# Optimization experiments

Hardware: AMD Instinct MI355X
Metric: run time of the kernel (lower is better)

The kernel has to match this reference:

```python
import jax, jax.numpy as jnp
import numpy as np
import math

N, NP, D, H, W, HEADS = 4, 1024, 256, 64, 64, 8
DH = D // HEADS


def _norm_coords(height, width):
    # (height*width, 2) with (x, y) in [0, 1], row-major flatten (y outer, x inner)
    y = jnp.linspace(0.0, 1.0, height)
    x = jnp.linspace(0.0, 1.0, width)
    yg, xg = jnp.meshgrid(y, x, indexing='ij')
    return jnp.stack([xg.reshape(-1), yg.reshape(-1)], axis=-1)


def _pos_enc(coords, dim):
    # coords: (P, 2) -> (P, dim); even slots sin(x*div), odd slots cos(y*div)
    div = jnp.exp(jnp.arange(0, dim, 2, dtype=coords.dtype) * (-math.log(10000.0) / dim))
    s = jnp.sin(coords[:, 0:1] * div)  # (P, dim/2)
    c = jnp.cos(coords[:, 1:2] * div)  # (P, dim/2)
    return jnp.stack([s, c], axis=-1).reshape(coords.shape[0], dim)


def setup_inputs() -> dict:
    key = jax.random.key(0)
    ks = jax.random.split(key, 10)
    sc = 1.0 / math.sqrt(D)
    return {
        "local_feat": jax.random.normal(ks[0], (N, NP, D), jnp.float32),
        "global_feat": jax.random.normal(ks[1], (N, D, H, W), jnp.float32),
        "Wq": jax.random.normal(ks[2], (D, D), jnp.float32) * sc,
        "bq": jax.random.normal(ks[3], (D,), jnp.float32) * sc,
        "Wk": jax.random.normal(ks[4], (D, D), jnp.float32) * sc,
        "bk": jax.random.normal(ks[5], (D,), jnp.float32) * sc,
        "Wv": jax.random.normal(ks[6], (D, D), jnp.float32) * sc,
        "bv": jax.random.normal(ks[7], (D,), jnp.float32) * sc,
        "Wo": jax.random.normal(ks[8], (D, D), jnp.float32) * sc,
        "bo": jax.random.normal(ks[9], (D,), jnp.float32) * sc,
    }


def reference(local_feat, global_feat, Wq, bq, Wk, bk, Wv, bv, Wo, bo):
    n, N_p, d = local_feat.shape
    _, _, h, w = global_feat.shape
    hw = h * w
    P = int(math.sqrt(N_p))

    gf = jnp.transpose(global_feat.reshape(n, d, hw), (0, 2, 1))  # (n, HW, d)

    lf = local_feat + _pos_enc(_norm_coords(P, P), d)[None]       # (n, N_p, d)
    gf = gf + _pos_enc(_norm_coords(h, w), d)[None]               # (n, HW, d)

    q = (lf @ Wq.T + bq).reshape(n, N_p, HEADS, DH)
    k = (gf @ Wk.T + bk).reshape(n, hw, HEADS, DH)
    v = (gf @ Wv.T + bv).reshape(n, hw, HEADS, DH)

    scores = jnp.einsum('bqhd,bkhd->bhqk', q, k) / math.sqrt(DH)  # (n, H, N_p, HW)
    attn = jax.nn.softmax(scores, axis=-1)
    out = jnp.einsum('bhqk,bkhd->bqhd', attn, v).reshape(n, N_p, d)

    return (lf + out) @ Wo.T + bo
```

## Files before the change

kernel.cpp:

```cpp
#include <hip/hip_runtime.h>
#include <hip/hip_bf16.h>
#include <math.h>

#define NB    4
#define NPTS  1024
#define DD    256
#define HWW   4096
#define NHEAD 8
#define DHD   32
#define VTROW 4128

typedef short s8v  __attribute__((ext_vector_type(8)));
typedef float f4v  __attribute__((ext_vector_type(4)));
typedef float f4s  __attribute__((ext_vector_type(4)));
typedef unsigned int u2v __attribute__((ext_vector_type(2)));
typedef unsigned int u4v __attribute__((ext_vector_type(4)));

#define MFMA_BF16 __builtin_amdgcn_mfma_f32_16x16x32_bf16

#define PE_FACT (-9.210340371976184f / 256.0f)
#define QSCALE 0.2550348637f

__device__ __forceinline__ unsigned packbf(float hi, float lo) {
    return __builtin_amdgcn_perm(__float_as_uint(hi), __float_as_uint(lo), 0x07060302u);
}
__device__ __forceinline__ unsigned pack2rne(float lo, float hi) {
    __hip_bfloat16 a = __float2bfloat16(lo), b = __float2bfloat16(hi);
    return (unsigned)*(unsigned short*)&a | ((unsigned)*(unsigned short*)&b << 16);
}

__global__ __launch_bounds__(256) void prep(const float* __restrict__ lf,
                                            const float* __restrict__ gfeat,
                                            const float* __restrict__ wq,
                                            const float* __restrict__ wk,
                                            const float* __restrict__ wv,
                                            const float* __restrict__ wo,
                                            __hip_bfloat16* __restrict__ lf_pe_b,
                                            __hip_bfloat16* __restrict__ gf_pe_b,
                                            __hip_bfloat16* __restrict__ W4) {
    __shared__ float tile[32][33];
    int b = blockIdx.x, tid = threadIdx.x;
    if (b < 1024) {
        int idx4 = (b * 256 + tid) * 4;
        f4s f = *(const f4s*)(lf + idx4);
        int c = idx4 & 255;
        int p = (idx4 >> 8) & 1023;
        float x = (float)(p & 31) * (1.0f / 31.0f);
        float y = (float)(p >> 5) * (1.0f / 31.0f);
        float div0 = __expf((float)c * PE_FACT);
        float div2 = __expf((float)(c + 2) * PE_FACT);
        float e0 = f.x + __sinf(x * div0);
        float e1 = f.y + __cosf(y * div0);
        float e2 = f.z + __sinf(x * div2);
        float e3 = f.w + __cosf(y * div2);
        u2v o2 = { pack2rne(e0, e1), pack2rne(e2, e3) };
        *(u2v*)((unsigned*)lf_pe_b + (idx4 >> 1)) = o2;
    } else if (b < 5120) {
        int t = b - 1024;
        int n = t >> 10, r = t & 1023;
        int p0 = (r >> 3) * 32, c0 = (r & 7) * 32;
        int tx = tid & 31, ty = tid >> 5;
#pragma unroll
        for (int i = 0; i < 4; ++i)
            tile[ty + 8 * i][tx] = gfeat[((size_t)n * DD + (c0 + ty + 8 * i)) * HWW + p0 + tx];
        __syncthreads();
#pragma unroll
        for (int i = 0; i < 4; ++i) {
            int p = p0 + ty + 8 * i, c = c0 + tx;
            float div = __expf((float)(c & ~1) * PE_FACT);
            float pe = (c & 1) ? __cosf((float)(p >> 6) * (1.0f / 63.0f) * div)
                               : __sinf((float)(p & 63) * (1.0f / 63.0f) * div);
            gf_pe_b[((size_t)n * HWW + p) * DD + c] = __float2bfloat16(tile[tx][ty + 8 * i] + pe);
        }
    } else {
        int idx4 = ((b - 5120) * 256 + tid) * 4;
        int m = idx4 >> 16, r = idx4 & 65535;
        const float* src = (m == 0) ? wq : (m == 1) ? wk : (m == 2) ? wv : wo;
        f4s f = *(const f4s*)(src + r);
        u2v o2 = { pack2rne(f.x, f.y), pack2rne(f.z, f.w) };
        *(u2v*)((unsigned*)W4 + (idx4 >> 1)) = o2;
    }
}

__global__ __launch_bounds__(256, 2) void gemmQKV(const __hip_bfloat16* __restrict__ Aq,
                                                  const __hip_bfloat16* __restrict__ Akv,
                                                  const __hip_bfloat16* __restrict__ W4,
                                                  const float* __restrict__ bq,
                                                  const float* __restrict__ bk,
                                                  const float* __restrict__ bv,
                                                  __hip_bfloat16* __restrict__ Qb,
                                                  __hip_bfloat16* __restrict__ Kb,
                                                  __hip_bfloat16* __restrict__ Vtb) {
    __shared__ __align__(16) unsigned shbuf[2304];
    int tid = threadIdx.x;
    int wave = tid >> 6, lane = tid & 63;
    int quad = lane >> 4, c16 = lane & 15;
    int b = blockIdx.x;

    int typ, c0, mgrp, mstride;
    const short* Ap;
    const short* Wp;
    const float* bias;
    if (b < 128) {
        typ = 0; c0 = (b >> 5) * 64; mgrp = b & 31; mstride = 2048;
        Ap = (const short*)Aq; Wp = (const short*)W4; bias = bq;
    } else {
        int bb = b - 128;
        int combo = bb >> 7;
        mgrp = bb & 127; mstride = 8192;
        int mat = combo & 1;
        typ = 1 + mat;
        c0 = (combo >> 1) * 64;
        Ap = (const short*)Akv;
        Wp = (const short*)W4 + (1 + mat) * DD * DD;
        bias = mat ? bv : bk;
    }

    s8v w[8][4];
    const short* wp0 = Wp + (c0 + c16) * DD + quad * 8;
#pragma unroll
    for (int ks = 0; ks < 8; ++ks)
#pragma unroll
        for (int t = 0; t < 4; ++t)
            w[ks][t] = *(const s8v*)(wp0 + t * 16 * DD + ks * 32);
    float bvv[4];
#pragma unroll
    for (int t = 0; t < 4; ++t) bvv[t] = bias[c0 + t * 16 + c16];

    int mbase0 = mgrp * 64;
    int mbase1 = mbase0 + mstride;
    const short* ap0 = Ap + (mbase0 + wave * 16 + c16) * DD + quad * 8;
    const short* ap1 = Ap + (mbase1 + wave * 16 + c16) * DD + quad * 8;
    s8v a0[8], a1[8];
#pragma unroll
    for (int ks = 0; ks < 8; ++ks) a0[ks] = *(const s8v*)(ap0 + ks * 32);
#pragma unroll
    for (int ks = 0; ks < 8; ++ks) a1[ks] = *(const s8v*)(ap1 + ks * 32);

#pragma unroll
    for (int it = 0; it < 2; ++it) {
        int mbase = it ? mbase1 : mbase0;
        f4v acc[4];
#pragma unroll
        for (int t = 0; t < 4; ++t) acc[t] = (f4v){0.f, 0.f, 0.f, 0.f};
#pragma unroll
        for (int ks = 0; ks < 8; ++ks) {
            s8v a = it ? a1[ks] : a0[ks];
#pragma unroll
            for (int t = 0; t < 4; ++t)
                acc[t] = MFMA_BF16(a, w[ks][t], acc[t], 0, 0, 0);
        }

        if (typ != 2) {
            short* kt = (short*)shbuf;
            __syncthreads();
#pragma unroll
            for (int t = 0; t < 4; ++t) {
#pragma unroll
                for (int r = 0; r < 4; ++r) {
                    float v = acc[t][r] + bvv[t];
                    if (typ == 0) v *= QSCALE;
                    __hip_bfloat16 hv = __float2bfloat16(v);
                    kt[(wave * 16 + quad * 4 + r) * 72 + t * 16 + c16] = *(short*)&hv;
                }
            }
            __syncthreads();
            int pl  = tid >> 2;
            int seg = tid & 3;
            const short* src = kt + pl * 72 + seg * 16;
            u4v w0 = *(const u4v*)(src);
            u4v w1 = *(const u4v*)(src + 8);
            int h   = (c0 >> 5) + (seg >> 1);
            int dh0 = (seg & 1) * 16;
            short* dst;
            if (typ == 0) {
                int row = mbase + pl;
                int n = row >> 10, p = row & 1023;
                dst = (short*)Qb + (((size_t)(n * NHEAD + h) << 10) + p) * DHD + dh0;
            } else {
                int n = mbase >> 12, p = (mbase & 4095) + pl;
                dst = (short*)Kb + (((size_t)(n * NHEAD + h) << 12) + p) * DHD + dh0;
            }
            *(u4v*)(dst)     = w0;
            *(u4v*)(dst + 8) = w1;
        } else {
            unsigned (*stv)[36] = (unsigned (*)[36])shbuf;
            __syncthreads();
#pragma unroll
            for (int t = 0; t < 4; ++t) {
#pragma unroll
                for (int rp = 0; rp < 2; ++rp) {
                    __hip_bfloat16 lo = __float2bfloat16(acc[t][2 * rp] + bvv[t]);
                    __hip_bfloat16 hi = __float2bfloat16(acc[t][2 * rp + 1] + bvv[t]);
                    unsigned dw = (unsigned)*(unsigned short*)&lo |
                                  ((unsigned)*(unsigned short*)&hi << 16);
                    stv[t * 16 + c16][wave * 8 + quad * 2 + rp] = dw;
                }
            }
            __syncthreads();
            int col = tid >> 2;
            int kd  = (tid & 3) * 8;
            int grp = kd & 16;
            int ob  = kd & 15;
            unsigned vals[8];
#pragma unroll
            for (int i = 0; i < 8; ++i) {
                int o = ob + i;
                int idw = ((o >> 2) << 1) | (o & 1) | ((o & 2) << 2);
                vals[i] = stv[col][grp + idw];
            }
            int nblk = mbase >> 12;
            int kb   = mbase & 4095;
            int gh = (c0 + col) >> 5, gdh = (c0 + col) & 31;
            short* vp = (short*)Vtb + ((size_t)(nblk * NHEAD + gh) * DHD + gdh) * VTROW + kb + kd * 2;
            *(u4v*)(vp)     = (u4v){vals[0], vals[1], vals[2], vals[3]};
            *(u4v*)(vp + 8) = (u4v){vals[4], vals[5], vals[6], vals[7]};
        }
    }
}

template <int NC>
__global__ __launch_bounds__(256) void attn(const __hip_bfloat16* __restrict__ Q,
                                            const __hip_bfloat16* __restrict__ Kg,
                                            const __hip_bfloat16* __restrict__ Vt,
                                            __hip_bfloat16* __restrict__ Opart,
                                            float* __restrict__ lpart) {
    constexpr int CK = HWW / NC;
    constexpr int NSTEP = CK / 32;

    int tid = threadIdx.x;
    int wave = tid >> 6, lane = tid & 63;
    int quad = lane >> 4, c16 = lane & 15;

    int id = blockIdx.x;
    int xcd = id & 7;
    int s = id >> 3;
    int qtile = s & 3;
    int gidx = ((s >> 2) << 3) | xcd;
    int bh = gidx & 31;
    int chunk = gidx >> 5;

    int q0 = qtile * 256 + wave * 64;

    const short* Qs = (const short*)Q + (size_t)bh * NPTS * DHD;
    const short* Ks = (const short*)Kg + ((size_t)bh * HWW + (size_t)chunk * CK) * DHD;
    const short* Vs = (const short*)Vt + (size_t)bh * DHD * VTROW + (size_t)chunk * CK;

    s8v aq[4];
#pragma unroll
    for (int g = 0; g < 4; ++g)
        aq[g] = *(const s8v*)(Qs + (q0 + g * 16 + c16) * DHD + quad * 8);

    const f4v zf = {0.f, 0.f, 0.f, 0.f};
    f4v o[4][2];
#pragma unroll
    for (int g = 0; g < 4; ++g) { o[g][0] = zf; o[g][1] = zf; }
    float lsum[4] = {0.f, 0.f, 0.f, 0.f};

    const short* kbase  = Ks + c16 * DHD + quad * 8;
    const short* v0base = Vs + c16 * VTROW + quad * 8;
    const short* v1base = Vs + (16 + c16) * VTROW + quad * 8;

    s8v kfA = *(const s8v*)(kbase);
    s8v kfB = *(const s8v*)(kbase + 16 * DHD);
    s8v vfA = *(const s8v*)(v0base);
    s8v vfB = *(const s8v*)(v1base);

    for (int st = 0; st < NSTEP; ++st) {
        bool more = (st + 1) < NSTEP;
        s8v nkA, nkB, nvA, nvB;
        if (more) {
            int ko = (st + 1) * 32;
            nkA = *(const s8v*)(kbase + ko * DHD);
            nkB = *(const s8v*)(kbase + ko * DHD + 16 * DHD);
            nvA = *(const s8v*)(v0base + ko);
            nvB = *(const s8v*)(v1base + ko);
        }
#pragma unroll
        for (int g = 0; g < 4; ++g) {
            f4v sA = MFMA_BF16(kfA, aq[g], zf, 0, 0, 0);
            f4v sB = MFMA_BF16(kfB, aq[g], zf, 0, 0, 0);
            float pA0 = __builtin_amdgcn_exp2f(sA[0]);
            float pA1 = __builtin_amdgcn_exp2f(sA[1]);
            float pA2 = __builtin_amdgcn_exp2f(sA[2]);
            float pA3 = __builtin_amdgcn_exp2f(sA[3]);
            float pB0 = __builtin_amdgcn_exp2f(sB[0]);
            float pB1 = __builtin_amdgcn_exp2f(sB[1]);
            float pB2 = __builtin_amdgcn_exp2f(sB[2]);
            float pB3 = __builtin_amdgcn_exp2f(sB[3]);
            lsum[g] += ((pA0 + pA1) + (pA2 + pA3)) + ((pB0 + pB1) + (pB2 + pB3));
            union { u4v u; s8v s; } pf;
            pf.u = (u4v){packbf(pA1, pA0), packbf(pA3, pA2),
                         packbf(pB1, pB0), packbf(pB3, pB2)};
            o[g][0] = MFMA_BF16(vfA, pf.s, o[g][0], 0, 0, 0);
            o[g][1] = MFMA_BF16(vfB, pf.s, o[g][1], 0, 0, 0);
        }
        if (more) { kfA = nkA; kfB = nkB; vfA = nvA; vfB = nvB; }
    }

    size_t obase = (size_t)(chunk * 32 + bh) * NPTS;
#pragma unroll
    for (int g = 0; g < 4; ++g) {
        float l = lsum[g];
        l += __shfl_xor(l, 16);
        l += __shfl_xor(l, 32);
        int q = q0 + g * 16 + c16;
        if (quad == 0) lpart[obase + q] = l;
        unsigned d0 = packbf(o[g][0][1], o[g][0][0]);
        unsigned d1 = packbf(o[g][0][3], o[g][0][2]);
        unsigned d2 = packbf(o[g][1][1], o[g][1][0]);
        unsigned d3 = packbf(o[g][1][3], o[g][1][2]);
        unsigned* op = (unsigned*)Opart + (obase + q) * (DHD / 2);
        *(u2v*)(op + 2 * quad)     = (u2v){d0, d1};
        *(u2v*)(op + 8 + 2 * quad) = (u2v){d2, d3};
    }
}

template <int NC>
__global__ __launch_bounds__(256) void combineO(const __hip_bfloat16* __restrict__ Opart,
                                                const float* __restrict__ lpart,
                                                const __hip_bfloat16* __restrict__ lf_pe,
                                                const __hip_bfloat16* __restrict__ Wo4,
                                                const float* __restrict__ bo,
                                                float* __restrict__ out) {
    __shared__ __align__(16) short al[16][264];
    int tid = threadIdx.x;
    int m0 = blockIdx.x * 16;
    {
        int rl  = tid >> 4;
        int seg = tid & 15;
        int h   = seg >> 1;
        int rg = m0 + rl;
        int n = rg >> 10, q = rg & 1023;
        size_t bhq = ((size_t)(n * NHEAD + h) << 10) + q;
        int dh0 = (seg & 1) * 16;
        float l = 0.f;
        float ov[16];
#pragma unroll
        for (int d = 0; d < 16; ++d) ov[d] = 0.f;
#pragma unroll
        for (int ch = 0; ch < NC; ++ch) {
            size_t base = (size_t)ch * 32 * NPTS + bhq;
            l += lpart[base];
            const unsigned* op = (const unsigned*)((const short*)Opart + base * DHD + dh0);
#pragma unroll
            for (int dw = 0; dw < 8; ++dw) {
                unsigned u = op[dw];
                ov[2 * dw]     += __uint_as_float(u << 16);
                ov[2 * dw + 1] += __uint_as_float(u & 0xffff0000u);
            }
        }
        float linv = 1.0f / l;
        const unsigned* lp = (const unsigned*)((const short*)lf_pe + ((size_t)rg * DD + seg * 16));
        unsigned* dst = (unsigned*)&al[rl][seg * 16];
#pragma unroll
        for (int dw = 0; dw < 8; ++dw) {
            unsigned u = lp[dw];
            float x0 = ov[2 * dw] * linv     + __uint_as_float(u << 16);
            float x1 = ov[2 * dw + 1] * linv + __uint_as_float(u & 0xffff0000u);
            dst[dw] = packbf(x1, x0);
        }
    }
    __syncthreads();
    int wave = tid >> 6, lane = tid & 63;
    int quad = lane >> 4, c16 = lane & 15;
    int ch0 = wave * 64;
    f4v acc[4];
#pragma unroll
    for (int t = 0; t < 4; ++t) acc[t] = (f4v){0.f, 0.f, 0.f, 0.f};
#pragma unroll
    for (int ks = 0; ks < 8; ++ks) {
        s8v af = *(const s8v*)&al[c16][ks * 32 + quad * 8];
#pragma unroll
        for (int t = 0; t < 4; ++t) {
            const short* wp = (const short*)Wo4 + (ch0 + t * 16 + c16) * DD + ks * 32 + quad * 8;
            s8v bf = *(const s8v*)wp;
            acc[t] = MFMA_BF16(af, bf, acc[t], 0, 0, 0);
        }
    }
#pragma unroll
    for (int t = 0; t < 4; ++t) {
        int col = ch0 + t * 16 + c16;
        float bv = bo[col];
#pragma unroll
        for (int r = 0; r < 4; ++r) {
            int row = m0 + quad * 4 + r;
            out[(size_t)row * DD + col] = acc[t][r] + bv;
        }
    }
}

extern "C" void kernel_launch(void* const* d_in, const int* in_sizes, int n_in,
                              void* d_out, int out_size, void* d_ws, size_t ws_size,
                              hipStream_t stream) {
    const float* lf    = (const float*)d_in[0];
    const float* gfeat = (const float*)d_in[1];
    const float* Wq    = (const float*)d_in[2];
    const float* bq    = (const float*)d_in[3];
    const float* Wk    = (const float*)d_in[4];
    const float* bk    = (const float*)d_in[5];
    const float* Wv    = (const float*)d_in[6];
    const float* bv    = (const float*)d_in[7];
    const float* Wo    = (const float*)d_in[8];
    const float* bo    = (const float*)d_in[9];

    const size_t MB = 1u << 20;
    char* ws = (char*)d_ws;
    __hip_bfloat16* lf_pe_b = (__hip_bfloat16*)(ws);
    __hip_bfloat16* gf_pe_b = (__hip_bfloat16*)(ws + 2 * MB);
    __hip_bfloat16* W4      = (__hip_bfloat16*)(ws + 10 * MB);
    __hip_bfloat16* Qb      = (__hip_bfloat16*)(ws + 10 * MB + 512 * 1024);
    __hip_bfloat16* Kb      = (__hip_bfloat16*)(ws + 12 * MB + 512 * 1024);
    __hip_bfloat16* Vtb     = (__hip_bfloat16*)(ws + 20 * MB + 512 * 1024);
    float*          lpart   = (float*)(ws + 31 * MB);
    __hip_bfloat16* Opart   = (__hip_bfloat16*)(ws + 32 * MB);

    prep<<<dim3(5376), dim3(256), 0, stream>>>(lf, gfeat, Wq, Wk, Wv, Wo,
                                               lf_pe_b, gf_pe_b, W4);
    gemmQKV<<<dim3(1152), dim3(256), 0, stream>>>(lf_pe_b, gf_pe_b, W4, bq, bk, bv,
                                                  Qb, Kb, Vtb);

    if (ws_size >= 48 * MB) {
        attn<8><<<dim3(128 * 8), dim3(256), 0, stream>>>(Qb, Kb, Vtb, Opart, lpart);
        combineO<8><<<dim3(256), dim3(256), 0, stream>>>(Opart, lpart, lf_pe_b,
                                                         W4 + 3 * DD * DD, bo, (float*)d_out);
    } else if (ws_size >= 40 * MB) {
        attn<4><<<dim3(128 * 4), dim3(256), 0, stream>>>(Qb, Kb, Vtb, Opart, lpart);
        combineO<4><<<dim3(256), dim3(256), 0, stream>>>(Opart, lpart, lf_pe_b,
                                                         W4 + 3 * DD * DD, bo, (float*)d_out);
    } else if (ws_size >= 36 * MB) {
        attn<2><<<dim3(128 * 2), dim3(256), 0, stream>>>(Qb, Kb, Vtb, Opart, lpart);
        combineO<2><<<dim3(256), dim3(256), 0, stream>>>(Opart, lpart, lf_pe_b,
                                                         W4 + 3 * DD * DD, bo, (float*)d_out);
    } else {
        attn<1><<<dim3(128 * 1), dim3(256), 0, stream>>>(Qb, Kb, Vtb, Opart, lpart);
        combineO<1><<<dim3(256), dim3(256), 0, stream>>>(Opart, lpart, lf_pe_b,
                                                         W4 + 3 * DD * DD, bo, (float*)d_out);
    }
}
```

Before: 159.3 us.

## Fuse attention with output projection and drop split-KV partial buffers

Replaces the split-KV attention kernel and the separate combine/output-projection kernel with one kernel. Each block handles 16 queries of one batch across all 8 heads (two heads per wave) over the full key range. It normalizes in registers, adds the positional-encoded local features in LDS, and runs the Wo projection directly. This removes the Opart/lpart round trip through memory and one launch. In exchange, each K/V fragment is reused by only one query group instead of four, so K/V load traffic doubles. Parallelism also drops to 256 blocks, each running a long serial loop over the keys.

```diff
diff --git a/kernel.cpp b/kernel.cpp
--- a/kernel.cpp
+++ b/kernel.cpp
@@ -219,67 +219,69 @@
     }
 }
 
-template <int NC>
-__global__ __launch_bounds__(256) void attn(const __hip_bfloat16* __restrict__ Q,
-                                            const __hip_bfloat16* __restrict__ Kg,
-                                            const __hip_bfloat16* __restrict__ Vt,
-                                            __hip_bfloat16* __restrict__ Opart,
-                                            float* __restrict__ lpart) {
-    constexpr int CK = HWW / NC;
-    constexpr int NSTEP = CK / 32;
-
+__global__ __launch_bounds__(256) void attnO(const __hip_bfloat16* __restrict__ Q,
+                                             const __hip_bfloat16* __restrict__ Kg,
+                                             const __hip_bfloat16* __restrict__ Vt,
+                                             const __hip_bfloat16* __restrict__ lf_pe,
+                                             const __hip_bfloat16* __restrict__ Wo4,
+                                             const float* __restrict__ bo,
+                                             float* __restrict__ out) {
+    __shared__ __align__(16) short al[16][264];
     int tid = threadIdx.x;
     int wave = tid >> 6, lane = tid & 63;
     int quad = lane >> 4, c16 = lane & 15;
 
     int id = blockIdx.x;
     int xcd = id & 7;
-    int s = id >> 3;
-    int qtile = s & 3;
-    int gidx = ((s >> 2) << 3) | xcd;
-    int bh = gidx & 31;
-    int chunk = gidx >> 5;
-
-    int q0 = qtile * 256 + wave * 64;
-
-    const short* Qs = (const short*)Q + (size_t)bh * NPTS * DHD;
-    const short* Ks = (const short*)Kg + ((size_t)bh * HWW + (size_t)chunk * CK) * DHD;
-    const short* Vs = (const short*)Vt + (size_t)bh * DHD * VTROW + (size_t)chunk * CK;
-
-    s8v aq[4];
-#pragma unroll
-    for (int g = 0; g < 4; ++g)
-        aq[g] = *(const s8v*)(Qs + (q0 + g * 16 + c16) * DHD + quad * 8);
+    int n = xcd & 3;
+    int qt = (id >> 3) + ((xcd >> 2) << 5);
+    int q0 = qt * 16;
 
     const f4v zf = {0.f, 0.f, 0.f, 0.f};
-    f4v o[4][2];
-#pragma unroll
-    for (int g = 0; g < 4; ++g) { o[g][0] = zf; o[g][1] = zf; }
-    float lsum[4] = {0.f, 0.f, 0.f, 0.f};
-
-    const short* kbase  = Ks + c16 * DHD + quad * 8;
-    const short* v0base = Vs + c16 * VTROW + quad * 8;
-    const short* v1base = Vs + (16 + c16) * VTROW + quad * 8;
-
-    s8v kfA = *(const s8v*)(kbase);
-    s8v kfB = *(const s8v*)(kbase + 16 * DHD);
-    s8v vfA = *(const s8v*)(v0base);
-    s8v vfB = *(const s8v*)(v1base);
-
-    for (int st = 0; st < NSTEP; ++st) {
-        bool more = (st + 1) < NSTEP;
-        s8v nkA, nkB, nvA, nvB;
+    const short* kbase[2];
+    const short* v0base[2];
+    const short* v1base[2];
+    s8v aq[2];
+#pragma unroll
+    for (int hh = 0; hh < 2; ++hh) {
+        int bh = n * NHEAD + wave * 2 + hh;
+        const short* Qs = (const short*)Q + (size_t)bh * NPTS * DHD;
+        aq[hh] = *(const s8v*)(Qs + (q0 + c16) * DHD + quad * 8);
+        kbase[hh]  = (const short*)Kg + (size_t)bh * HWW * DHD + c16 * DHD + quad * 8;
+        v0base[hh] = (const short*)Vt + (size_t)bh * DHD * VTROW + c16 * VTROW + quad * 8;
+        v1base[hh] = v0base[hh] + 16 * VTROW;
+    }
+
+    f4v o[2][2];
+    o[0][0] = zf; o[0][1] = zf; o[1][0] = zf; o[1][1] = zf;
+    float lsum[2] = {0.f, 0.f};
+
+    s8v kfA[2], kfB[2], vfA[2], vfB[2];
+#pragma unroll
+    for (int hh = 0; hh < 2; ++hh) {
+        kfA[hh] = *(const s8v*)(kbase[hh]);
+        kfB[hh] = *(const s8v*)(kbase[hh] + 16 * DHD);
+        vfA[hh] = *(const s8v*)(v0base[hh]);
+        vfB[hh] = *(const s8v*)(v1base[hh]);
+    }
+
+    for (int st = 0; st < HWW / 32; ++st) {
+        bool more = (st + 1) < HWW / 32;
+        s8v nkA[2], nkB[2], nvA[2], nvB[2];
         if (more) {
             int ko = (st + 1) * 32;
-            nkA = *(const s8v*)(kbase + ko * DHD);
-            nkB = *(const s8v*)(kbase + ko * DHD + 16 * DHD);
-            nvA = *(const s8v*)(v0base + ko);
-            nvB = *(const s8v*)(v1base + ko);
-        }
-#pragma unroll
-        for (int g = 0; g < 4; ++g) {
-            f4v sA = MFMA_BF16(kfA, aq[g], zf, 0, 0, 0);
-            f4v sB = MFMA_BF16(kfB, aq[g], zf, 0, 0, 0);
+#pragma unroll
+            for (int hh = 0; hh < 2; ++hh) {
+                nkA[hh] = *(const s8v*)(kbase[hh] + ko * DHD);
+                nkB[hh] = *(const s8v*)(kbase[hh] + ko * DHD + 16 * DHD);
+                nvA[hh] = *(const s8v*)(v0base[hh] + ko);
+                nvB[hh] = *(const s8v*)(v1base[hh] + ko);
+            }
+        }
+#pragma unroll
+        for (int hh = 0; hh < 2; ++hh) {
+            f4v sA = MFMA_BF16(kfA[hh], aq[hh], zf, 0, 0, 0);
+            f4v sB = MFMA_BF16(kfB[hh], aq[hh], zf, 0, 0, 0);
             float pA0 = __builtin_amdgcn_exp2f(sA[0]);
             float pA1 = __builtin_amdgcn_exp2f(sA[1]);
             float pA2 = __builtin_amdgcn_exp2f(sA[2]);
@@ -288,82 +290,49 @@
             float pB1 = __builtin_amdgcn_exp2f(sB[1]);
             float pB2 = __builtin_amdgcn_exp2f(sB[2]);
             float pB3 = __builtin_amdgcn_exp2f(sB[3]);
-            lsum[g] += ((pA0 + pA1) + (pA2 + pA3)) + ((pB0 + pB1) + (pB2 + pB3));
+            lsum[hh] += ((pA0 + pA1) + (pA2 + pA3)) + ((pB0 + pB1) + (pB2 + pB3));
             union { u4v u; s8v s; } pf;
             pf.u = (u4v){packbf(pA1, pA0), packbf(pA3, pA2),
                          packbf(pB1, pB0), packbf(pB3, pB2)};
-            o[g][0] = MFMA_BF16(vfA, pf.s, o[g][0], 0, 0, 0);
-            o[g][1] = MFMA_BF16(vfB, pf.s, o[g][1], 0, 0, 0);
-        }
-        if (more) { kfA = nkA; kfB = nkB; vfA = nvA; vfB = nvB; }
-    }
-
-    size_t obase = (size_t)(chunk * 32 + bh) * NPTS;
-#pragma unroll
-    for (int g = 0; g < 4; ++g) {
-        float l = lsum[g];
+            o[hh][0] = MFMA_BF16(vfA[hh], pf.s, o[hh][0], 0, 0, 0);
+            o[hh][1] = MFMA_BF16(vfB[hh], pf.s, o[hh][1], 0, 0, 0);
+        }
+        if (more) {
+#pragma unroll
+            for (int hh = 0; hh < 2; ++hh) {
+                kfA[hh] = nkA[hh]; kfB[hh] = nkB[hh];
+                vfA[hh] = nvA[hh]; vfB[hh] = nvB[hh];
+            }
+        }
+    }
+
+    {
+        int rl = tid >> 4, sg = tid & 15;
+        const short* srcp = (const short*)lf_pe + ((size_t)(n * NPTS + q0 + rl)) * DD + sg * 16;
+        *(u4v*)&al[rl][sg * 16]     = *(const u4v*)(srcp);
+        *(u4v*)&al[rl][sg * 16 + 8] = *(const u4v*)(srcp + 8);
+    }
+    __syncthreads();
+#pragma unroll
+    for (int hh = 0; hh < 2; ++hh) {
+        float l = lsum[hh];
         l += __shfl_xor(l, 16);
         l += __shfl_xor(l, 32);
-        int q = q0 + g * 16 + c16;
-        if (quad == 0) lpart[obase + q] = l;
-        unsigned d0 = packbf(o[g][0][1], o[g][0][0]);
-        unsigned d1 = packbf(o[g][0][3], o[g][0][2]);
-        unsigned d2 = packbf(o[g][1][1], o[g][1][0]);
-        unsigned d3 = packbf(o[g][1][3], o[g][1][2]);
-        unsigned* op = (unsigned*)Opart + (obase + q) * (DHD / 2);
-        *(u2v*)(op + 2 * quad)     = (u2v){d0, d1};
-        *(u2v*)(op + 8 + 2 * quad) = (u2v){d2, d3};
-    }
-}
-
-template <int NC>
-__global__ __launch_bounds__(256) void combineO(const __hip_bfloat16* __restrict__ Opart,
-                                                const float* __restrict__ lpart,
-                                                const __hip_bfloat16* __restrict__ lf_pe,
-                                                const __hip_bfloat16* __restrict__ Wo4,
-                                                const float* __restrict__ bo,
-                                                float* __restrict__ out) {
-    __shared__ __align__(16) short al[16][264];
-    int tid = threadIdx.x;
-    int m0 = blockIdx.x * 16;
-    {
-        int rl  = tid >> 4;
-        int seg = tid & 15;
-        int h   = seg >> 1;
-        int rg = m0 + rl;
-        int n = rg >> 10, q = rg & 1023;
-        size_t bhq = ((size_t)(n * NHEAD + h) << 10) + q;
-        int dh0 = (seg & 1) * 16;
-        float l = 0.f;
-        float ov[16];
-#pragma unroll
-        for (int d = 0; d < 16; ++d) ov[d] = 0.f;
-#pragma unroll
-        for (int ch = 0; ch < NC; ++ch) {
-            size_t base = (size_t)ch * 32 * NPTS + bhq;
-            l += lpart[base];
-            const unsigned* op = (const unsigned*)((const short*)Opart + base * DHD + dh0);
-#pragma unroll
-            for (int dw = 0; dw < 8; ++dw) {
-                unsigned u = op[dw];
-                ov[2 * dw]     += __uint_as_float(u << 16);
-                ov[2 * dw + 1] += __uint_as_float(u & 0xffff0000u);
-            }
-        }
         float linv = 1.0f / l;
-        const unsigned* lp = (const unsigned*)((const short*)lf_pe + ((size_t)rg * DD + seg * 16));
-        unsigned* dst = (unsigned*)&al[rl][seg * 16];
-#pragma unroll
-        for (int dw = 0; dw < 8; ++dw) {
-            unsigned u = lp[dw];
-            float x0 = ov[2 * dw] * linv     + __uint_as_float(u << 16);
-            float x1 = ov[2 * dw + 1] * linv + __uint_as_float(u & 0xffff0000u);
-            dst[dw] = packbf(x1, x0);
+        int cb = (wave * 2 + hh) * 32;
+#pragma unroll
+        for (int half = 0; half < 2; ++half) {
+#pragma unroll
+            for (int r = 0; r < 4; ++r) {
+                int col = cb + half * 16 + quad * 4 + r;
+                __hip_bfloat16* slot = (__hip_bfloat16*)&al[c16][col];
+                float v = __bfloat162float(*slot) + o[hh][half][r] * linv;
+                *slot = __float2bfloat16(v);
+            }
         }
     }
     __syncthreads();
-    int wave = tid >> 6, lane = tid & 63;
-    int quad = lane >> 4, c16 = lane & 15;
+    int m0 = n * NPTS + q0;
     int ch0 = wave * 64;
     f4v acc[4];
 #pragma unroll
@@ -412,29 +381,11 @@
     __hip_bfloat16* Qb      = (__hip_bfloat16*)(ws + 10 * MB + 512 * 1024);
     __hip_bfloat16* Kb      = (__hip_bfloat16*)(ws + 12 * MB + 512 * 1024);
     __hip_bfloat16* Vtb     = (__hip_bfloat16*)(ws + 20 * MB + 512 * 1024);
-    float*          lpart   = (float*)(ws + 31 * MB);
-    __hip_bfloat16* Opart   = (__hip_bfloat16*)(ws + 32 * MB);
 
     prep<<<dim3(5376), dim3(256), 0, stream>>>(lf, gfeat, Wq, Wk, Wv, Wo,
                                                lf_pe_b, gf_pe_b, W4);
     gemmQKV<<<dim3(1152), dim3(256), 0, stream>>>(lf_pe_b, gf_pe_b, W4, bq, bk, bv,
                                                   Qb, Kb, Vtb);
-
-    if (ws_size >= 48 * MB) {
-        attn<8><<<dim3(128 * 8), dim3(256), 0, stream>>>(Qb, Kb, Vtb, Opart, lpart);
-        combineO<8><<<dim3(256), dim3(256), 0, stream>>>(Opart, lpart, lf_pe_b,
-                                                         W4 + 3 * DD * DD, bo, (float*)d_out);
-    } else if (ws_size >= 40 * MB) {
-        attn<4><<<dim3(128 * 4), dim3(256), 0, stream>>>(Qb, Kb, Vtb, Opart, lpart);
-        combineO<4><<<dim3(256), dim3(256), 0, stream>>>(Opart, lpart, lf_pe_b,
-                                                         W4 + 3 * DD * DD, bo, (float*)d_out);
-    } else if (ws_size >= 36 * MB) {
-        attn<2><<<dim3(128 * 2), dim3(256), 0, stream>>>(Qb, Kb, Vtb, Opart, lpart);
-        combineO<2><<<dim3(256), dim3(256), 0, stream>>>(Opart, lpart, lf_pe_b,
-                                                         W4 + 3 * DD * DD, bo, (float*)d_out);
-    } else {
-        attn<1><<<dim3(128 * 1), dim3(256), 0, stream>>>(Qb, Kb, Vtb, Opart, lpart);
-        combineO<1><<<dim3(256), dim3(256), 0, stream>>>(Opart, lpart, lf_pe_b,
-                                                         W4 + 3 * DD * DD, bo, (float*)d_out);
-    }
-}
+    attnO<<<dim3(256), dim3(256), 0, stream>>>(Qb, Kb, Vtb, lf_pe_b,
+                                               W4 + 3 * DD * DD, bo, (float*)d_out);
+}
```

After: 196.6 us. 23.5% more time.
